# Kernel optimization log

Hardware: AMD Instinct MI355X
Metric: run time of the kernel (lower is better)

Reference implementation:

```python
import jax, jax.numpy as jnp
import numpy as np

B, T, I, H = 64, 2048, 256, 256


def setup_inputs() -> dict:
    key = jax.random.key(0)
    ks = jax.random.split(key, 6)
    s = 1.0 / np.sqrt(H)
    x = jax.random.normal(ks[0], (B, T, I), dtype=jnp.float32)
    att_weights = jax.random.uniform(ks[1], (B, T), dtype=jnp.float32)
    lengths = jax.random.randint(ks[2], (B,), 1, T + 1, dtype=jnp.int32)
    W_ih = jax.random.uniform(ks[3], (3 * H, I), minval=-s, maxval=s, dtype=jnp.float32)
    W_hh = jax.random.uniform(ks[4], (3 * H, H), minval=-s, maxval=s, dtype=jnp.float32)
    b_ih = jax.random.uniform(ks[5], (3 * H,), minval=-s, maxval=s, dtype=jnp.float32)
    b_hh = jax.random.uniform(jax.random.fold_in(key, 7), (3 * H,), minval=-s, maxval=s, dtype=jnp.float32)
    return {"x": x, "att_weights": att_weights, "lengths": lengths,
            "W_ih": W_ih, "W_hh": W_hh, "b_ih": b_ih, "b_hh": b_hh}


def reference(x, att_weights, lengths, W_ih, W_hh, b_ih, b_hh):
    # x: [B, T, I]; att_weights: [B, T]; lengths: [B]
    Bv, Tv, _ = x.shape
    Hv = W_hh.shape[1]
    # Padded equivalent of the packed-sequence loop: update h only while t < length.
    mask = jnp.arange(Tv)[None, :] < lengths[:, None]  # [B, T]

    def step(h, inp):
        xt, wt, mt = inp  # [B, I], [B], [B]
        gi = xt @ W_ih.T + b_ih  # [B, 3H]
        gh = h @ W_hh.T + b_hh   # [B, 3H]
        i_r, i_z, i_n = jnp.split(gi, 3, axis=-1)
        h_r, h_z, h_n = jnp.split(gh, 3, axis=-1)
        r = jax.nn.sigmoid(i_r + h_r)
        z = jax.nn.sigmoid(i_z + h_z)
        n = jnp.tanh(i_n + r * h_n)
        h_new = (1.0 - z) * n + z * h  # GRUCell output
        w = wt[:, None]
        h_gated = w * h_new + (1.0 - w) * h  # attention gating
        h = jnp.where(mt[:, None], h_gated, h)
        return h, None

    h0 = jnp.zeros((Bv, Hv), dtype=x.dtype)
    xs = (jnp.swapaxes(x, 0, 1), att_weights.T, mask.T)  # time-major
    hT, _ = jax.lax.scan(step, h0, xs)
    return hT  # [B, H]
```

## Files before the change

### kernel.cpp

```cpp
#include <hip/hip_runtime.h>
#include <stdint.h>

#define B_ 64
#define T_ 2048
#define I_ 256
#define H_ 256
#define G3 768
#define NPROD 192
#define CH 16
#define NTILE_N 6

typedef _Float16 half2v __attribute__((ext_vector_type(2)));
typedef _Float16 half8v __attribute__((ext_vector_type(8)));

#if __has_builtin(__builtin_amdgcn_fdot2)
#define FDOT2(a, b, c) __builtin_amdgcn_fdot2((a), (b), (c), false)
#else
#define FDOT2(a, b, c) fmaf((float)(a)[1], (float)(b)[1], fmaf((float)(a)[0], (float)(b)[0], (c)))
#endif

#define BAR_LGKM() do {                      \
    __builtin_amdgcn_s_waitcnt(0xC07F);      \
    __builtin_amdgcn_s_barrier();            \
  } while (0)

__global__ void zero_flags(int* __restrict__ done, int n)
{
  int i = threadIdx.x + blockIdx.x * blockDim.x;
  if (i < n) __hip_atomic_store(&done[i], 0, __ATOMIC_RELAXED, __HIP_MEMORY_SCOPE_AGENT);
}

__global__ __launch_bounds__(512) __attribute__((amdgpu_waves_per_eu(2, 2)))
void fused(const float* __restrict__ x, const float* __restrict__ att,
           const int* __restrict__ lengths, const float* __restrict__ Wih,
           const float* __restrict__ Whh, const float* __restrict__ bih,
           const float* __restrict__ bhh, float* __restrict__ gi,
           int* __restrict__ done, float* __restrict__ hws,
           float* __restrict__ out, int t0, int t1)
{
  __shared__ __align__(16) float smem[32 * 68 + 32 * 132];
  const int tid = threadIdx.x;
  const int Tc = t1 - t0;

  if (blockIdx.x >= B_) {
    const int pid = blockIdx.x - B_;
    float* As = smem;
    float* Bs = smem + 32 * 68;
    const int ty = tid >> 5, tx = tid & 31;
    const int lr = tid >> 3;
    const int lk = (tid & 7) << 2;
    const int NT = Tc * NTILE_N;
    for (int i = pid; i < NT; i += NPROD) {
      const int rel = i / NTILE_N;
      const int tt  = t0 + rel;
      const int n0  = (i % NTILE_N) << 7;
      float acc[4][4] = {};
      for (int kc = 0; kc < I_; kc += 32) {
        float4 a0 = *(const float4*)(x + ((size_t)lr * T_ + tt) * I_ + kc + lk);
        float4 b0 = *(const float4*)(Wih + (size_t)(n0 + lr) * I_ + kc + lk);
        float4 b1 = *(const float4*)(Wih + (size_t)(n0 + lr + 64) * I_ + kc + lk);
        __syncthreads();
        As[(lk + 0) * 68 + lr] = a0.x; As[(lk + 1) * 68 + lr] = a0.y;
        As[(lk + 2) * 68 + lr] = a0.z; As[(lk + 3) * 68 + lr] = a0.w;
        Bs[(lk + 0) * 132 + lr] = b0.x; Bs[(lk + 1) * 132 + lr] = b0.y;
        Bs[(lk + 2) * 132 + lr] = b0.z; Bs[(lk + 3) * 132 + lr] = b0.w;
        Bs[(lk + 0) * 132 + lr + 64] = b1.x; Bs[(lk + 1) * 132 + lr + 64] = b1.y;
        Bs[(lk + 2) * 132 + lr + 64] = b1.z; Bs[(lk + 3) * 132 + lr + 64] = b1.w;
        __syncthreads();
        #pragma unroll
        for (int kk = 0; kk < 32; ++kk) {
          float4 av = *(const float4*)(&As[kk * 68 + (ty << 2)]);
          float4 bv = *(const float4*)(&Bs[kk * 132 + (tx << 2)]);
          float av_[4] = {av.x, av.y, av.z, av.w};
          float bv_[4] = {bv.x, bv.y, bv.z, bv.w};
          #pragma unroll
          for (int u = 0; u < 4; ++u)
            #pragma unroll
            for (int v = 0; v < 4; ++v)
              acc[u][v] = fmaf(av_[u], bv_[v], acc[u][v]);
        }
      }
      const int colb = n0 + (tx << 2);
      float4 bi = *(const float4*)(bih + colb);
      float4 bh = *(const float4*)(bhh + colb);
      float4 badd;
      badd.x = bi.x + (colb + 0 < 512 ? bh.x : 0.f);
      badd.y = bi.y + (colb + 1 < 512 ? bh.y : 0.f);
      badd.z = bi.z + (colb + 2 < 512 ? bh.z : 0.f);
      badd.w = bi.w + (colb + 3 < 512 ? bh.w : 0.f);
      float* gout = gi + (size_t)rel * B_ * G3;
      #pragma unroll
      for (int r = 0; r < 4; ++r) {
        const int bb = (ty << 2) + r;
        float4 o;
        o.x = acc[r][0] + badd.x; o.y = acc[r][1] + badd.y;
        o.z = acc[r][2] + badd.z; o.w = acc[r][3] + badd.w;
        *(float4*)(gout + (size_t)bb * G3 + colb) = o;
      }
      __syncthreads();
      if (tid == 0) {
        __threadfence();
        __hip_atomic_fetch_add(&done[rel >> 4], 1, __ATOMIC_RELEASE, __HIP_MEMORY_SCOPE_AGENT);
      }
    }
    return;
  }

  const int b  = blockIdx.x;
  const int j  = tid >> 1;
  const int s  = tid & 1;
  const int k0 = s << 7;
  _Float16* hbuf  = (_Float16*)smem;
  float*    att_s = smem + 384;

  half2v w[192];
  #pragma unroll
  for (int g = 0; g < 3; ++g) {
    const float* row = Whh + (size_t)(g * 256 + j) * H_ + k0;
    #pragma unroll
    for (int q = 0; q < 32; ++q) {
      float4 v = *(const float4*)(row + (q << 2));
      half2v a, c;
      a[0] = (_Float16)v.x; a[1] = (_Float16)v.y;
      c[0] = (_Float16)v.z; c[1] = (_Float16)v.w;
      w[g * 64 + 2 * q]     = a;
      w[g * 64 + 2 * q + 1] = c;
    }
  }

  float bhn = 0.f, h_reg = 0.f;
  if (s == 0) {
    bhn = bhh[512 + j];
    h_reg = (t0 > 0) ? hws[b * H_ + j] : 0.f;
  }
  if (tid < 256) {
    float v = (t0 > 0) ? hws[b * H_ + tid] : 0.f;
    hbuf[(tid >> 7) * 136 + (tid & 127)] = (_Float16)v;
  }
  for (int i = tid; i < Tc; i += 512) att_s[i] = att[(size_t)b * T_ + t0 + i];
  int len = lengths[b]; if (len > t1) len = t1;
  const int nch = (Tc + CH - 1) / CH;
  int wm = -1;
  __syncthreads();

#define GATE(NEED) do {                                                               \
    int need_ = (NEED); if (need_ > nch - 1) need_ = nch - 1;                         \
    if (need_ > wm) {                                                                 \
      if (tid == 0) {                                                                 \
        for (int c_ = wm + 1; c_ <= need_; ++c_) {                                    \
          int exp_ = ((Tc - c_ * CH) < CH ? (Tc - c_ * CH) : CH) * NTILE_N;           \
          while (__hip_atomic_load(&done[c_], __ATOMIC_RELAXED,                       \
                                   __HIP_MEMORY_SCOPE_AGENT) < exp_)                  \
            __builtin_amdgcn_s_sleep(2);                                              \
        }                                                                             \
      }                                                                               \
      __syncthreads();                                                                \
      __threadfence();       \
      wm = need_;                                                                     \
    }                                                                                 \
  } while (0)

#define STEP(GR, GZ, GN, TT, ISSUE_OK) do {                                           \
    float wat_ = (s == 0) ? att_s[(TT) - t0] : 0.f;                                   \
    float accr = 0.f, accz = 0.f, accn = 0.f;                                         \
    const _Float16* hb = hbuf + p * 272 + s * 136;                                    \
    _Pragma("unroll")                                                                 \
    for (int q = 0; q < 16; ++q) {                                                    \
      half8v hv = *(const half8v*)(hb + (q << 3));                                    \
      half2v h0_ = __builtin_shufflevector(hv, hv, 0, 1);                             \
      half2v h1_ = __builtin_shufflevector(hv, hv, 2, 3);                             \
      half2v h2_ = __builtin_shufflevector(hv, hv, 4, 5);                             \
      half2v h3_ = __builtin_shufflevector(hv, hv, 6, 7);                             \
      const int qq = q << 2;                                                          \
      accr = FDOT2(w[qq + 0], h0_, accr);                                             \
      accr = FDOT2(w[qq + 1], h1_, accr);                                             \
      accr = FDOT2(w[qq + 2], h2_, accr);                                             \
      accr = FDOT2(w[qq + 3], h3_, accr);                                             \
      accz = FDOT2(w[64 + qq + 0], h0_, accz);                                        \
      accz = FDOT2(w[64 + qq + 1], h1_, accz);                                        \
      accz = FDOT2(w[64 + qq + 2], h2_, accz);                                        \
      accz = FDOT2(w[64 + qq + 3], h3_, accz);                                        \
      accn = FDOT2(w[128 + qq + 0], h0_, accn);                                       \
      accn = FDOT2(w[128 + qq + 1], h1_, accn);                                       \
      accn = FDOT2(w[128 + qq + 2], h2_, accn);                                       \
      accn = FDOT2(w[128 + qq + 3], h3_, accn);                                       \
    }                                                                                 \
    accr += __shfl_xor(accr, 1);                                                      \
    accz += __shfl_xor(accz, 1);                                                      \
    accn += __shfl_xor(accn, 1);                                                      \
    if (s == 0) {                                                                     \
      float r_ = 1.f / (1.f + __expf(-(accr + GR)));                                  \
      float z_ = 1.f / (1.f + __expf(-(accz + GZ)));                                  \
      float e2_ = __expf(2.f * (GN + r_ * (accn + bhn)));                             \
      float nn_ = 1.f - 2.f / (e2_ + 1.f);                                            \
      float hnew_ = (1.f - z_) * nn_ + z_ * h_reg;                                    \
      h_reg = wat_ * hnew_ + (1.f - wat_) * h_reg;                                    \
      hbuf[(p ^ 1) * 272 + (j >> 7) * 136 + (j & 127)] = (_Float16)h_reg;             \
    }                                                                                 \
    if (s == 0 && (ISSUE_OK)) {                      \
      const float* gb_ = gi + ((size_t)((TT) + 4 - t0) * B_ + b) * G3;                \
      GR = gb_[j]; GZ = gb_[256 + j]; GN = gb_[512 + j];                              \
    }                                                                                 \
    BAR_LGKM();                                                                       \
    p ^= 1;                                                                           \
  } while (0)

  GATE(0);
  float a_gr = 0.f, a_gz = 0.f, a_gn = 0.f;
  float b_gr = 0.f, b_gz = 0.f, b_gn = 0.f;
  float c_gr = 0.f, c_gz = 0.f, c_gn = 0.f;
  float d_gr = 0.f, d_gz = 0.f, d_gn = 0.f;
  if (s == 0 && t0 + 0 < len) {
    const float* gb = gi + ((size_t)0 * B_ + b) * G3;
    a_gr = gb[j]; a_gz = gb[256 + j]; a_gn = gb[512 + j];
  }
  if (s == 0 && t0 + 1 < len) {
    const float* gb = gi + ((size_t)1 * B_ + b) * G3;
    b_gr = gb[j]; b_gz = gb[256 + j]; b_gn = gb[512 + j];
  }
  if (s == 0 && t0 + 2 < len) {
    const float* gb = gi + ((size_t)2 * B_ + b) * G3;
    c_gr = gb[j]; c_gz = gb[256 + j]; c_gn = gb[512 + j];
  }
  if (s == 0 && t0 + 3 < len) {
    const float* gb = gi + ((size_t)3 * B_ + b) * G3;
    d_gr = gb[j]; d_gz = gb[256 + j]; d_gn = gb[512 + j];
  }

  int p = 0;
  int t = t0;
  for (; t + 3 < len; t += 4) {
    GATE((t + 7 - t0) >> 4);
    STEP(a_gr, a_gz, a_gn, t,     (t + 4 < len));
    STEP(b_gr, b_gz, b_gn, t + 1, (t + 5 < len));
    STEP(c_gr, c_gz, c_gn, t + 2, (t + 6 < len));
    STEP(d_gr, d_gz, d_gn, t + 3, (t + 7 < len));
  }
  if (t < len) { STEP(a_gr, a_gz, a_gn, t, false); ++t; }
  if (t < len) { STEP(b_gr, b_gz, b_gn, t, false); ++t; }
  if (t < len) { STEP(c_gr, c_gz, c_gn, t, false); ++t; }

  if (s == 0) {
    hws[b * H_ + j] = h_reg;
    if (t1 == T_) out[b * H_ + j] = h_reg;
  }
#undef STEP
#undef GATE
}

extern "C" void kernel_launch(void* const* d_in, const int* in_sizes, int n_in,
                              void* d_out, int out_size, void* d_ws, size_t ws_size,
                              hipStream_t stream)
{
  const float* x       = (const float*)d_in[0];
  const float* att     = (const float*)d_in[1];
  const int*   lengths = (const int*)d_in[2];
  const float* Wih     = (const float*)d_in[3];
  const float* Whh     = (const float*)d_in[4];
  const float* bih     = (const float*)d_in[5];
  const float* bhh     = (const float*)d_in[6];
  float* out = (float*)d_out;

  int*   done = (int*)d_ws;
  float* hws  = (float*)((char*)d_ws + 4096);
  float* gi   = (float*)((char*)d_ws + 4096 + 65536);
  const size_t used0 = 4096 + 65536;
  const size_t per_t = (size_t)B_ * G3 * sizeof(float);
  size_t avail = ws_size > used0 ? ws_size - used0 : 0;
  int Tc = (int)(avail / per_t);
  if (Tc > T_) Tc = T_;
  if (Tc < 1) Tc = 1;

  for (int t0 = 0; t0 < T_; t0 += Tc) {
    int t1 = t0 + Tc; if (t1 > T_) t1 = T_;
    int nch = (t1 - t0 + CH - 1) / CH;
    zero_flags<<<dim3((nch + 127) / 128), 128, 0, stream>>>(done, nch);
    fused<<<dim3(B_ + NPROD), 512, 0, stream>>>(x, att, lengths, Wih, Whh, bih, bhh,
                                                gi, done, hws, out, t0, t1);
  }
}
```

Measured before the change: 3.710 ms.

## Split recurrent dot products four ways with two hidden units per thread

Each thread now owns two hidden units (j0 and j0+128) and a quarter of the K dimension, where before it owned one unit and half of K. Each step's dot product becomes half as long, with a two-stage xor shuffle reduction, and the gate math is done twice per owning lane. The padded shared hidden-state layout changes to match. The input-gate prefetch depth drops from four steps to three to free registers. The aim is to shorten the serial per-step critical path, at the cost of more shuffles and more serialized gate math on a quarter of the lanes.

New measurement: 4.154 ms. 12.0% more time.

```diff
diff --git a/kernel.cpp b/kernel.cpp
--- a/kernel.cpp
+++ b/kernel.cpp
@@ -107,35 +107,40 @@
   }
 
   const int b  = blockIdx.x;
-  const int j  = tid >> 1;
-  const int s  = tid & 1;
-  const int k0 = s << 7;
+  const int j0 = tid >> 2;
+  const int s2 = tid & 3;
+  const int k0 = s2 << 6;
   _Float16* hbuf  = (_Float16*)smem;
-  float*    att_s = smem + 384;
+  float*    att_s = smem + 288;
 
   half2v w[192];
   #pragma unroll
   for (int g = 0; g < 3; ++g) {
-    const float* row = Whh + (size_t)(g * 256 + j) * H_ + k0;
     #pragma unroll
-    for (int q = 0; q < 32; ++q) {
-      float4 v = *(const float4*)(row + (q << 2));
-      half2v a, c;
-      a[0] = (_Float16)v.x; a[1] = (_Float16)v.y;
-      c[0] = (_Float16)v.z; c[1] = (_Float16)v.w;
-      w[g * 64 + 2 * q]     = a;
-      w[g * 64 + 2 * q + 1] = c;
+    for (int c = 0; c < 2; ++c) {
+      const float* row = Whh + (size_t)(g * 256 + j0 + 128 * c) * H_ + k0;
+      const int base = (g * 2 + c) * 32;
+      #pragma unroll
+      for (int q = 0; q < 16; ++q) {
+        float4 v = *(const float4*)(row + (q << 2));
+        half2v a, cc;
+        a[0]  = (_Float16)v.x; a[1]  = (_Float16)v.y;
+        cc[0] = (_Float16)v.z; cc[1] = (_Float16)v.w;
+        w[base + 2 * q]     = a;
+        w[base + 2 * q + 1] = cc;
+      }
     }
   }
 
-  float bhn = 0.f, h_reg = 0.f;
-  if (s == 0) {
-    bhn = bhh[512 + j];
-    h_reg = (t0 > 0) ? hws[b * H_ + j] : 0.f;
+  float bhnA = 0.f, bhnB = 0.f, hA = 0.f, hB = 0.f;
+  if (s2 == 0) {
+    bhnA = bhh[512 + j0];
+    bhnB = bhh[512 + 128 + j0];
+    if (t0 > 0) { hA = hws[b * H_ + j0]; hB = hws[b * H_ + 128 + j0]; }
   }
   if (tid < 256) {
     float v = (t0 > 0) ? hws[b * H_ + tid] : 0.f;
-    hbuf[(tid >> 7) * 136 + (tid & 127)] = (_Float16)v;
+    hbuf[(tid >> 6) * 72 + (tid & 63)] = (_Float16)v;
   }
   for (int i = tid; i < Tc; i += 512) att_s[i] = att[(size_t)b * T_ + t0 + i];
   int len = lengths[b]; if (len > t1) len = t1;
@@ -160,89 +165,111 @@
     }                                                                                 \
   } while (0)
 
-#define STEP(GR, GZ, GN, TT, ISSUE_OK) do {                                           \
-    float wat_ = (s == 0) ? att_s[(TT) - t0] : 0.f;                                   \
-    float accr = 0.f, accz = 0.f, accn = 0.f;                                         \
-    const _Float16* hb = hbuf + p * 272 + s * 136;                                    \
+#define STEP(GRA, GZA, GNA, GRB, GZB, GNB, TT, ISSUE_OK) do {                         \
+    float wat_ = (s2 == 0) ? att_s[(TT) - t0] : 0.f;                                  \
+    float arA = 0.f, azA = 0.f, anA = 0.f;                                            \
+    float arB = 0.f, azB = 0.f, anB = 0.f;                                            \
+    const _Float16* hb = hbuf + p * 288 + s2 * 72;                                    \
     _Pragma("unroll")                                                                 \
-    for (int q = 0; q < 16; ++q) {                                                    \
+    for (int q = 0; q < 8; ++q) {                                                     \
       half8v hv = *(const half8v*)(hb + (q << 3));                                    \
       half2v h0_ = __builtin_shufflevector(hv, hv, 0, 1);                             \
       half2v h1_ = __builtin_shufflevector(hv, hv, 2, 3);                             \
       half2v h2_ = __builtin_shufflevector(hv, hv, 4, 5);                             \
       half2v h3_ = __builtin_shufflevector(hv, hv, 6, 7);                             \
       const int qq = q << 2;                                                          \
-      accr = FDOT2(w[qq + 0], h0_, accr);                                             \
-      accr = FDOT2(w[qq + 1], h1_, accr);                                             \
-      accr = FDOT2(w[qq + 2], h2_, accr);                                             \
-      accr = FDOT2(w[qq + 3], h3_, accr);                                             \
-      accz = FDOT2(w[64 + qq + 0], h0_, accz);                                        \
-      accz = FDOT2(w[64 + qq + 1], h1_, accz);                                        \
-      accz = FDOT2(w[64 + qq + 2], h2_, accz);                                        \
-      accz = FDOT2(w[64 + qq + 3], h3_, accz);                                        \
-      accn = FDOT2(w[128 + qq + 0], h0_, accn);                                       \
-      accn = FDOT2(w[128 + qq + 1], h1_, accn);                                       \
-      accn = FDOT2(w[128 + qq + 2], h2_, accn);                                       \
-      accn = FDOT2(w[128 + qq + 3], h3_, accn);                                       \
+      arA = FDOT2(w[qq + 0], h0_, arA);                                               \
+      arA = FDOT2(w[qq + 1], h1_, arA);                                               \
+      arA = FDOT2(w[qq + 2], h2_, arA);                                               \
+      arA = FDOT2(w[qq + 3], h3_, arA);                                               \
+      arB = FDOT2(w[32 + qq + 0], h0_, arB);                                          \
+      arB = FDOT2(w[32 + qq + 1], h1_, arB);                                          \
+      arB = FDOT2(w[32 + qq + 2], h2_, arB);                                          \
+      arB = FDOT2(w[32 + qq + 3], h3_, arB);                                          \
+      azA = FDOT2(w[64 + qq + 0], h0_, azA);                                          \
+      azA = FDOT2(w[64 + qq + 1], h1_, azA);                                          \
+      azA = FDOT2(w[64 + qq + 2], h2_, azA);                                          \
+      azA = FDOT2(w[64 + qq + 3], h3_, azA);                                          \
+      azB = FDOT2(w[96 + qq + 0], h0_, azB);                                          \
+      azB = FDOT2(w[96 + qq + 1], h1_, azB);                                          \
+      azB = FDOT2(w[96 + qq + 2], h2_, azB);                                          \
+      azB = FDOT2(w[96 + qq + 3], h3_, azB);                                          \
+      anA = FDOT2(w[128 + qq + 0], h0_, anA);                                         \
+      anA = FDOT2(w[128 + qq + 1], h1_, anA);                                         \
+      anA = FDOT2(w[128 + qq + 2], h2_, anA);                                         \
+      anA = FDOT2(w[128 + qq + 3], h3_, anA);                                         \
+      anB = FDOT2(w[160 + qq + 0], h0_, anB);                                         \
+      anB = FDOT2(w[160 + qq + 1], h1_, anB);                                         \
+      anB = FDOT2(w[160 + qq + 2], h2_, anB);                                         \
+      anB = FDOT2(w[160 + qq + 3], h3_, anB);                                         \
     }                                                                                 \
-    accr += __shfl_xor(accr, 1);                                                      \
-    accz += __shfl_xor(accz, 1);                                                      \
-    accn += __shfl_xor(accn, 1);                                                      \
-    if (s == 0) {                                                                     \
-      float r_ = 1.f / (1.f + __expf(-(accr + GR)));                                  \
-      float z_ = 1.f / (1.f + __expf(-(accz + GZ)));                                  \
-      float e2_ = __expf(2.f * (GN + r_ * (accn + bhn)));                             \
-      float nn_ = 1.f - 2.f / (e2_ + 1.f);                                            \
-      float hnew_ = (1.f - z_) * nn_ + z_ * h_reg;                                    \
-      h_reg = wat_ * hnew_ + (1.f - wat_) * h_reg;                                    \
-      hbuf[(p ^ 1) * 272 + (j >> 7) * 136 + (j & 127)] = (_Float16)h_reg;             \
+    arA += __shfl_xor(arA, 1); arA += __shfl_xor(arA, 2);                             \
+    azA += __shfl_xor(azA, 1); azA += __shfl_xor(azA, 2);                             \
+    anA += __shfl_xor(anA, 1); anA += __shfl_xor(anA, 2);                             \
+    arB += __shfl_xor(arB, 1); arB += __shfl_xor(arB, 2);                             \
+    azB += __shfl_xor(azB, 1); azB += __shfl_xor(azB, 2);                             \
+    anB += __shfl_xor(anB, 1); anB += __shfl_xor(anB, 2);                             \
+    if (s2 == 0) {                                                                    \
+      float rA = 1.f / (1.f + __expf(-(arA + GRA)));                                  \
+      float zA = 1.f / (1.f + __expf(-(azA + GZA)));                                  \
+      float e2A = __expf(2.f * (GNA + rA * (anA + bhnA)));                            \
+      float nnA = 1.f - 2.f / (e2A + 1.f);                                            \
+      float hnA = (1.f - zA) * nnA + zA * hA;                                         \
+      hA = wat_ * hnA + (1.f - wat_) * hA;                                            \
+      float rB = 1.f / (1.f + __expf(-(arB + GRB)));                                  \
+      float zB = 1.f / (1.f + __expf(-(azB + GZB)));                                  \
+      float e2B = __expf(2.f * (GNB + rB * (anB + bhnB)));                            \
+      float nnB = 1.f - 2.f / (e2B + 1.f);                                            \
+      float hnB = (1.f - zB) * nnB + zB * hB;                                         \
+      hB = wat_ * hnB + (1.f - wat_) * hB;                                            \
+      const int pp = (p ^ 1) * 288;                                                   \
+      hbuf[pp + (j0 >> 6) * 72 + (j0 & 63)]       = (_Float16)hA;                     \
+      hbuf[pp + 144 + (j0 >> 6) * 72 + (j0 & 63)] = (_Float16)hB;                     \
     }                                                                                 \
-    if (s == 0 && (ISSUE_OK)) {                      \
-      const float* gb_ = gi + ((size_t)((TT) + 4 - t0) * B_ + b) * G3;                \
-      GR = gb_[j]; GZ = gb_[256 + j]; GN = gb_[512 + j];                              \
+    if (s2 == 0 && (ISSUE_OK)) {                     \
+      const float* gb_ = gi + ((size_t)((TT) + 3 - t0) * B_ + b) * G3;                \
+      GRA = gb_[j0];       GZA = gb_[256 + j0];       GNA = gb_[512 + j0];            \
+      GRB = gb_[128 + j0]; GZB = gb_[384 + j0];       GNB = gb_[640 + j0];            \
     }                                                                                 \
     BAR_LGKM();                                                                       \
     p ^= 1;                                                                           \
   } while (0)
 
   GATE(0);
-  float a_gr = 0.f, a_gz = 0.f, a_gn = 0.f;
-  float b_gr = 0.f, b_gz = 0.f, b_gn = 0.f;
-  float c_gr = 0.f, c_gz = 0.f, c_gn = 0.f;
-  float d_gr = 0.f, d_gz = 0.f, d_gn = 0.f;
-  if (s == 0 && t0 + 0 < len) {
+  float A_gr = 0.f, A_gz = 0.f, A_gn = 0.f, A_hr = 0.f, A_hz = 0.f, A_hn = 0.f;
+  float B_gr = 0.f, B_gz = 0.f, B_gn = 0.f, B_hr = 0.f, B_hz = 0.f, B_hn = 0.f;
+  float C_gr = 0.f, C_gz = 0.f, C_gn = 0.f, C_hr = 0.f, C_hz = 0.f, C_hn = 0.f;
+  if (s2 == 0 && t0 + 0 < len) {
     const float* gb = gi + ((size_t)0 * B_ + b) * G3;
-    a_gr = gb[j]; a_gz = gb[256 + j]; a_gn = gb[512 + j];
-  }
-  if (s == 0 && t0 + 1 < len) {
+    A_gr = gb[j0]; A_gz = gb[256 + j0]; A_gn = gb[512 + j0];
+    A_hr = gb[128 + j0]; A_hz = gb[384 + j0]; A_hn = gb[640 + j0];
+  }
+  if (s2 == 0 && t0 + 1 < len) {
     const float* gb = gi + ((size_t)1 * B_ + b) * G3;
-    b_gr = gb[j]; b_gz = gb[256 + j]; b_gn = gb[512 + j];
-  }
-  if (s == 0 && t0 + 2 < len) {
+    B_gr = gb[j0]; B_gz = gb[256 + j0]; B_gn = gb[512 + j0];
+    B_hr = gb[128 + j0]; B_hz = gb[384 + j0]; B_hn = gb[640 + j0];
+  }
+  if (s2 == 0 && t0 + 2 < len) {
     const float* gb = gi + ((size_t)2 * B_ + b) * G3;
-    c_gr = gb[j]; c_gz = gb[256 + j]; c_gn = gb[512 + j];
-  }
-  if (s == 0 && t0 + 3 < len) {
-    const float* gb = gi + ((size_t)3 * B_ + b) * G3;
-    d_gr = gb[j]; d_gz = gb[256 + j]; d_gn = gb[512 + j];
+    C_gr = gb[j0]; C_gz = gb[256 + j0]; C_gn = gb[512 + j0];
+    C_hr = gb[128 + j0]; C_hz = gb[384 + j0]; C_hn = gb[640 + j0];
   }
 
   int p = 0;
   int t = t0;
-  for (; t + 3 < len; t += 4) {
-    GATE((t + 7 - t0) >> 4);
-    STEP(a_gr, a_gz, a_gn, t,     (t + 4 < len));
-    STEP(b_gr, b_gz, b_gn, t + 1, (t + 5 < len));
-    STEP(c_gr, c_gz, c_gn, t + 2, (t + 6 < len));
-    STEP(d_gr, d_gz, d_gn, t + 3, (t + 7 < len));
-  }
-  if (t < len) { STEP(a_gr, a_gz, a_gn, t, false); ++t; }
-  if (t < len) { STEP(b_gr, b_gz, b_gn, t, false); ++t; }
-  if (t < len) { STEP(c_gr, c_gz, c_gn, t, false); ++t; }
-
-  if (s == 0) {
-    hws[b * H_ + j] = h_reg;
-    if (t1 == T_) out[b * H_ + j] = h_reg;
+  for (; t + 2 < len; t += 3) {
+    GATE((t + 5 - t0) >> 4);
+    STEP(A_gr, A_gz, A_gn, A_hr, A_hz, A_hn, t,     (t + 3 < len));
+    STEP(B_gr, B_gz, B_gn, B_hr, B_hz, B_hn, t + 1, (t + 4 < len));
+    STEP(C_gr, C_gz, C_gn, C_hr, C_hz, C_hn, t + 2, (t + 5 < len));
+  }
+  if (t < len) { STEP(A_gr, A_gz, A_gn, A_hr, A_hz, A_hn, t, false); ++t; }
+  if (t < len) { STEP(B_gr, B_gz, B_gn, B_hr, B_hz, B_hn, t, false); ++t; }
+
+  if (s2 == 0) {
+    hws[b * H_ + j0]       = hA;
+    hws[b * H_ + 128 + j0] = hB;
+    if (t1 == T_) { out[b * H_ + j0] = hA; out[b * H_ + 128 + j0] = hB; }
   }
 #undef STEP
 #undef GATE
```
